# Kernel tuning notes

Hardware: AMD Instinct MI355X
Metric: run time of the kernel (lower is better)

Reference implementation:

```python
import jax, jax.numpy as jnp
import numpy as np

H, D = 2, 64          # heads, hidden_dim per head
HD = H * D            # 128
N_NODES = 50000
N_EDGES = 800000
N_GRAPHS = 64
IN_CH, EDGE_DIM, N_CLASSES = 2, 1, 30


def _tconv(x, src, dst, Wq, bq, Wk, bk, Wv, bv, We, Ws, bs):
    """PyG TransformerConv (concat=True, root_weight=True, beta=False)."""
    n = x.shape[0]
    q = (x @ Wq + bq).reshape(n, H, D)
    k = (x @ Wk + bk).reshape(n, H, D)
    v = (x @ Wv + bv).reshape(n, H, D)
    # edge embedding (lin_edge has no bias in PyG)
    return _attend(q, k, v, x @ Ws + bs, src, dst, We, n)


def _attend(q, k, v, skip, src, dst, We_e, n):
    kj = k[src] + We_e            # [E,H,D]
    vj = v[src] + We_e
    logits = (q[dst] * kj).sum(-1) / jnp.sqrt(jnp.asarray(D, q.dtype))  # [E,H]
    m = jax.ops.segment_max(logits, dst, num_segments=n)
    m = jnp.where(jnp.isfinite(m), m, jnp.zeros_like(m))
    ex = jnp.exp(logits - m[dst])
    denom = jax.ops.segment_sum(ex, dst, num_segments=n)
    alpha = ex / (denom[dst] + 1e-16)                                   # segment softmax
    agg = jax.ops.segment_sum(alpha[..., None] * vj, dst, num_segments=n)
    return agg.reshape(n, HD) + skip


def _forward(x, edge_index, edge_attr, batch,
             l0_Wq, l0_bq, l0_Wk, l0_bk, l0_Wv, l0_bv, l0_We, l0_Ws, l0_bs,
             l1_Wq, l1_bq, l1_Wk, l1_bk, l1_Wv, l1_bv, l1_We, l1_Ws, l1_bs,
             cW1, cb1, cW2, cb2):
    src, dst = edge_index[0], edge_index[1]
    e0 = (edge_attr @ l0_We).reshape(-1, H, D)
    e1 = (edge_attr @ l1_We).reshape(-1, H, D)
    n = x.shape[0]

    h = _attend((x @ l0_Wq + l0_bq).reshape(n, H, D),
                (x @ l0_Wk + l0_bk).reshape(n, H, D),
                (x @ l0_Wv + l0_bv).reshape(n, H, D),
                x @ l0_Ws + l0_bs, src, dst, e0, n)
    h = jax.nn.relu(h)
    h = _attend((h @ l1_Wq + l1_bq).reshape(n, H, D),
                (h @ l1_Wk + l1_bk).reshape(n, H, D),
                (h @ l1_Wv + l1_bv).reshape(n, H, D),
                h @ l1_Ws + l1_bs, src, dst, e1, n)
    h = jax.nn.relu(h)

    # global_mean_pool over graphs
    sums = jax.ops.segment_sum(h, batch, num_segments=N_GRAPHS)
    cnt = jax.ops.segment_sum(jnp.ones((n,), h.dtype), batch, num_segments=N_GRAPHS)
    g = sums / jnp.maximum(cnt, 1.0)[:, None]                           # [G, 128]

    return jax.nn.relu(g @ cW1 + cb1) @ cW2 + cb2                       # [G, 30]


def setup_inputs() -> dict:
    key = jax.random.key(0)
    ks = jax.random.split(key, 40)
    it = iter(ks)

    def lin(k, fan_in, fan_out):
        s = 1.0 / np.sqrt(fan_in)
        return jax.random.uniform(k, (fan_in, fan_out), jnp.float32, -s, s)

    inp = {
        'x': jax.random.normal(next(it), (N_NODES, IN_CH), jnp.float32),
        'edge_index': jax.random.randint(next(it), (2, N_EDGES), 0, N_NODES),
        'edge_attr': jax.random.normal(next(it), (N_EDGES, EDGE_DIM), jnp.float32),
        'batch': jnp.sort(jax.random.randint(next(it), (N_NODES,), 0, N_GRAPHS)),
    }
    for li, cin in (('l0', IN_CH), ('l1', HD)):
        for nm in ('Wq', 'Wk', 'Wv'):
            inp[f'{li}_{nm}'] = lin(next(it), cin, HD)
            inp[f'{li}_{nm.replace("W", "b")}'] = jax.random.uniform(
                next(it), (HD,), jnp.float32, -1 / np.sqrt(cin), 1 / np.sqrt(cin))
        inp[f'{li}_We'] = lin(next(it), EDGE_DIM, HD)
        inp[f'{li}_Ws'] = lin(next(it), cin, HD)
        inp[f'{li}_bs'] = jax.random.uniform(next(it), (HD,), jnp.float32,
                                             -1 / np.sqrt(cin), 1 / np.sqrt(cin))
    inp['cW1'] = lin(next(it), HD, 128)
    inp['cb1'] = jax.random.uniform(next(it), (128,), jnp.float32, -1 / np.sqrt(HD), 1 / np.sqrt(HD))
    inp['cW2'] = lin(next(it), 128, N_CLASSES)
    inp['cb2'] = jax.random.uniform(next(it), (N_CLASSES,), jnp.float32, -1 / np.sqrt(128), 1 / np.sqrt(128))
    return inp


def reference(x, edge_index, edge_attr, batch,
              l0_Wq, l0_bq, l0_Wk, l0_bk, l0_Wv, l0_bv, l0_We, l0_Ws, l0_bs,
              l1_Wq, l1_bq, l1_Wk, l1_bk, l1_Wv, l1_bv, l1_We, l1_Ws, l1_bs,
              cW1, cb1, cW2, cb2):
    return _forward(x, edge_index, edge_attr, batch,
                    l0_Wq, l0_bq, l0_Wk, l0_bk, l0_Wv, l0_bv, l0_We, l0_Ws, l0_bs,
                    l1_Wq, l1_bq, l1_Wk, l1_bk, l1_Wv, l1_bv, l1_We, l1_Ws, l1_bs,
                    cW1, cb1, cW2, cb2)
```

## Files before the change

### kernel.cpp

```cpp
#include <hip/hip_runtime.h>
#include <hip/hip_fp16.h>
#include <cstdint>
#include <cstddef>

#define HD 128

typedef short bf16x8 __attribute__((ext_vector_type(8)));
typedef float f32x4 __attribute__((ext_vector_type(4)));

__device__ __forceinline__ unsigned short f2bf(float f) {
    unsigned int u = __float_as_uint(f);
    u += 0x7fff + ((u >> 16) & 1);
    return (unsigned short)(u >> 16);
}
__device__ __forceinline__ float bf2f(unsigned short h) {
    return __uint_as_float(((unsigned int)h) << 16);
}

template<int CTRL>
__device__ __forceinline__ float dpp_add(float x) {
    int y = __builtin_amdgcn_update_dpp(0, __float_as_int(x), CTRL, 0xF, 0xF, true);
    return x + __int_as_float(y);
}
__device__ __forceinline__ float half_reduce(float x) {
    x = dpp_add<0xB1>(x);
    x = dpp_add<0x4E>(x);
    x = dpp_add<0x124>(x);
    x = dpp_add<0x128>(x);
    x += __shfl_xor(x, 16, 64);
    return x;
}

__device__ __forceinline__ void pair_update_s(
    float& m, float& s, float2& acc,
    float lA, float lB,
    float vAx, float vAy, float vBx, float vBy)
{
    float nm = fmaxf(fmaxf(m, lA), lB);
    float sc = __expf(m - nm);
    float eA = __expf(lA - nm);
    float eB = __expf(lB - nm);
    s     = fmaf(s, sc, eA + eB);
    acc.x = fmaf(acc.x, sc, fmaf(eA, vAx, eB * vBx));
    acc.y = fmaf(acc.y, sc, fmaf(eA, vAy, eB * vBy));
    m = nm;
}
__device__ __forceinline__ void single_update_s(
    float& m, float& s, float2& acc,
    float lg, float vx, float vy)
{
    float nm = fmaxf(m, lg);
    float sc = __expf(m - nm);
    float ex = __expf(lg - nm);
    s     = fmaf(s, sc, ex);
    acc.x = fmaf(acc.x, sc, ex * vx);
    acc.y = fmaf(acc.y, sc, ex * vy);
    m = nm;
}

__global__ __launch_bounds__(256) void hist_kernel(
    const int* __restrict__ dst, int* __restrict__ cnt, int E)
{
    int e = blockIdx.x * 256 + threadIdx.x;
    if (e < E) atomicAdd(&cnt[dst[e]], 1);
}

__global__ __launch_bounds__(256) void scanA_kernel(
    const int* __restrict__ cnt, int* __restrict__ row_ptr,
    int* __restrict__ bsum, int n)
{
    __shared__ int sdata[256];
    int t = threadIdx.x;
    int base = blockIdx.x * 512 + 2 * t;
    int a = (base < n) ? cnt[base] : 0;
    int b = (base + 1 < n) ? cnt[base + 1] : 0;
    int local = a + b;
    sdata[t] = local;
    __syncthreads();
    #pragma unroll
    for (int off = 1; off < 256; off <<= 1) {
        int val = (t >= off) ? sdata[t - off] : 0;
        __syncthreads();
        sdata[t] += val;
        __syncthreads();
    }
    int excl = sdata[t] - local;
    if (base < n)     row_ptr[base] = excl;
    if (base + 1 < n) row_ptr[base + 1] = excl + a;
    if (t == 255) bsum[blockIdx.x] = sdata[255];
}

__global__ __launch_bounds__(256) void scanB_kernel(
    const int* __restrict__ bsum, int* __restrict__ boff, int B)
{
    __shared__ int sdata[256];
    int t = threadIdx.x;
    int local = (t < B) ? bsum[t] : 0;
    sdata[t] = local;
    __syncthreads();
    #pragma unroll
    for (int off = 1; off < 256; off <<= 1) {
        int val = (t >= off) ? sdata[t - off] : 0;
        __syncthreads();
        sdata[t] += val;
        __syncthreads();
    }
    if (t < B) boff[t] = sdata[t] - local;
}

__global__ __launch_bounds__(256) void scanC_kernel(
    int* __restrict__ row_ptr, int* __restrict__ cursor,
    const int* __restrict__ boff, int n, int E)
{
    int t = threadIdx.x;
    int base = blockIdx.x * 512 + 2 * t;
    int off = boff[blockIdx.x];
    if (base + 1 < n) {
        int2 v = *(int2*)&row_ptr[base];
        v.x += off; v.y += off;
        *(int2*)&row_ptr[base] = v;
        *(int2*)&cursor[base]  = v;
    } else if (base < n) {
        int v = row_ptr[base] + off;
        row_ptr[base] = v; cursor[base] = v;
    }
    if (blockIdx.x == 0 && t == 0) row_ptr[n] = E;
}

__global__ __launch_bounds__(256) void scatter_kernel(
    const int* __restrict__ dst, const int* __restrict__ src,
    const float* __restrict__ eattr, int* __restrict__ cursor,
    int2* __restrict__ epack, int E)
{
    int e = blockIdx.x * 256 + threadIdx.x;
    if (e < E) {
        int pos = atomicAdd(&cursor[dst[e]], 1);
        epack[pos] = make_int2(src[e], __float_as_int(eattr[e]));
    }
}

__global__ __launch_bounds__(256) void attn0_kernel(
    const float* __restrict__ x,
    const float* __restrict__ Wq, const float* __restrict__ bq,
    const float* __restrict__ Wk, const float* __restrict__ bk,
    const float* __restrict__ Wv, const float* __restrict__ bv,
    const float* __restrict__ We, const float* __restrict__ Ws,
    const float* __restrict__ bs,
    const int2* __restrict__ epack, const int* __restrict__ row_ptr,
    float* __restrict__ out, int n)
{
    int i = blockIdx.x * 4 + (threadIdx.x >> 6);
    if (i >= n) return;
    int l = threadIdx.x & 63;
    int j0 = 2 * l;

    float2 wk0 = *(const float2*)&Wk[j0];
    float2 wk1 = *(const float2*)&Wk[HD + j0];
    float2 wv0 = *(const float2*)&Wv[j0];
    float2 wv1 = *(const float2*)&Wv[HD + j0];
    float2 bk2 = *(const float2*)&bk[j0];
    float2 bv2 = *(const float2*)&bv[j0];
    float2 we  = *(const float2*)&We[j0];

    float x0 = x[2 * i], x1 = x[2 * i + 1];
    float2 wq0 = *(const float2*)&Wq[j0];
    float2 wq1 = *(const float2*)&Wq[HD + j0];
    float2 bq2 = *(const float2*)&bq[j0];
    float2 q;
    q.x = fmaf(x1, wq1.x, fmaf(x0, wq0.x, bq2.x));
    q.y = fmaf(x1, wq1.y, fmaf(x0, wq0.y, bq2.y));

    float c0 = half_reduce(fmaf(q.x, wk0.x, q.y * wk0.y)) * 0.125f;
    float c1 = half_reduce(fmaf(q.x, wk1.x, q.y * wk1.y)) * 0.125f;
    float cb = half_reduce(fmaf(q.x, bk2.x, q.y * bk2.y)) * 0.125f;
    float cw = half_reduce(fmaf(q.x, we.x,  q.y * we.y))  * 0.125f;

    int p0 = __builtin_amdgcn_readfirstlane(row_ptr[i]);
    int p1 = __builtin_amdgcn_readfirstlane(row_ptr[i + 1]);

    float m = -INFINITY, s = 0.f;
    float2 acc = make_float2(0.f, 0.f);

    float2 xs0 = {}, xs1 = {}, xs2 = {}, xs3 = {};
    float ea0 = 0.f, ea1 = 0.f, ea2 = 0.f, ea3 = 0.f;

#define LD0(t, idx) do { if ((idx) < p1) { int2 ep_ = epack[idx]; \
    ea##t = __int_as_float(ep_.y); xs##t = *(const float2*)&x[2 * ep_.x]; } } while (0)

#define LOGIT0(xs, ea) fmaf(ea, cw, fmaf(xs.y, c1, fmaf(xs.x, c0, cb)))
#define VREC(xs, ea, vx, vy) \
    float vx = fmaf(ea, we.x, fmaf(xs.y, wv1.x, fmaf(xs.x, wv0.x, bv2.x))); \
    float vy = fmaf(ea, we.y, fmaf(xs.y, wv1.y, fmaf(xs.x, wv0.y, bv2.y)));

    LD0(0, p0); LD0(1, p0 + 1); LD0(2, p0 + 2); LD0(3, p0 + 3);

    int p = p0;
    for (; p + 3 < p1; p += 4) {
        float2 c0v = xs0, c1v = xs1, c2v = xs2, c3v = xs3;
        float a0 = ea0, a1 = ea1, a2 = ea2, a3 = ea3;
        LD0(0, p + 4); LD0(1, p + 5); LD0(2, p + 6); LD0(3, p + 7);
        { VREC(c0v, a0, vAx, vAy) VREC(c1v, a1, vBx, vBy)
          pair_update_s(m, s, acc, LOGIT0(c0v, a0), LOGIT0(c1v, a1), vAx, vAy, vBx, vBy); }
        { VREC(c2v, a2, vAx, vAy) VREC(c3v, a3, vBx, vBy)
          pair_update_s(m, s, acc, LOGIT0(c2v, a2), LOGIT0(c3v, a3), vAx, vAy, vBx, vBy); }
    }
    int rem = p1 - p;
    if (rem >= 2) {
        VREC(xs0, ea0, vAx, vAy) VREC(xs1, ea1, vBx, vBy)
        pair_update_s(m, s, acc, LOGIT0(xs0, ea0), LOGIT0(xs1, ea1), vAx, vAy, vBx, vBy);
    }
    if (rem == 1) {
        VREC(xs0, ea0, vx, vy)
        single_update_s(m, s, acc, LOGIT0(xs0, ea0), vx, vy);
    } else if (rem == 3) {
        VREC(xs2, ea2, vx, vy)
        single_update_s(m, s, acc, LOGIT0(xs2, ea2), vx, vy);
    }

    float inv = 1.f / (s + 1e-16f);
    float2 ws0 = *(const float2*)&Ws[j0];
    float2 ws1 = *(const float2*)&Ws[HD + j0];
    float2 bs2 = *(const float2*)&bs[j0];
    float sk_x = fmaf(x1, ws1.x, fmaf(x0, ws0.x, bs2.x));
    float sk_y = fmaf(x1, ws1.y, fmaf(x0, ws0.y, bs2.y));
    float2 res;
    res.x = fmaxf(fmaf(acc.x, inv, sk_x), 0.f);
    res.y = fmaxf(fmaf(acc.y, inv, sk_y), 0.f);
    *(float2*)&out[(size_t)i * HD + j0] = res;
}

__global__ __launch_bounds__(256) void attn_kernel(
    const __half* __restrict__ qh, const __half* __restrict__ kvh,
    const __half* __restrict__ sh, const float* __restrict__ We,
    const int2* __restrict__ epack, const int* __restrict__ row_ptr,
    float* __restrict__ out, int n)
{
    int i = blockIdx.x * 4 + (threadIdx.x >> 6);
    if (i >= n) return;
    int l = threadIdx.x & 63;
    const int2* kv8 = (const int2*)kvh;
    const __half2* qh2 = (const __half2*)qh;
    const __half2* sh2 = (const __half2*)sh;
    float2 q  = __half22float2(qh2[(size_t)i * 64 + l]);
    float2 we = *(const float2*)&We[2 * l];
    int p0 = __builtin_amdgcn_readfirstlane(row_ptr[i]);
    int p1 = __builtin_amdgcn_readfirstlane(row_ptr[i + 1]);

    float m = -INFINITY, s = 0.f;
    float2 acc = make_float2(0.f, 0.f);

    int2 kv0 = {}, kv1 = {}, kv2 = {}, kv3 = {};
    float ea0 = 0.f, ea1 = 0.f, ea2 = 0.f, ea3 = 0.f;

#define LD1(t, idx) do { if ((idx) < p1) { int2 ep_ = epack[idx]; \
    ea##t = __int_as_float(ep_.y); kv##t = kv8[(size_t)ep_.x * 64 + l]; } } while (0)

#define KVX(raw, ea, kx, ky, vx, vy) \
    float2 kf_##kx = __half22float2(*(const __half2*)&raw.x); \
    float2 vf_##kx = __half22float2(*(const __half2*)&raw.y); \
    float kx = fmaf(ea, we.x, kf_##kx.x), ky = fmaf(ea, we.y, kf_##kx.y); \
    float vx = fmaf(ea, we.x, vf_##kx.x), vy = fmaf(ea, we.y, vf_##kx.y);

    LD1(0, p0); LD1(1, p0 + 1); LD1(2, p0 + 2); LD1(3, p0 + 3);

    int p = p0;
    for (; p + 3 < p1; p += 4) {
        int2 c0 = kv0, c1 = kv1, c2 = kv2, c3 = kv3;
        float a0 = ea0, a1 = ea1, a2 = ea2, a3 = ea3;
        LD1(0, p + 4); LD1(1, p + 5); LD1(2, p + 6); LD1(3, p + 7);
        {
            KVX(c0, a0, kAx, kAy, vAx, vAy)
            KVX(c1, a1, kBx, kBy, vBx, vBy)
            float lA = half_reduce(fmaf(q.x, kAx, q.y * kAy)) * 0.125f;
            float lB = half_reduce(fmaf(q.x, kBx, q.y * kBy)) * 0.125f;
            pair_update_s(m, s, acc, lA, lB, vAx, vAy, vBx, vBy);
        }
        {
            KVX(c2, a2, kAx, kAy, vAx, vAy)
            KVX(c3, a3, kBx, kBy, vBx, vBy)
            float lA = half_reduce(fmaf(q.x, kAx, q.y * kAy)) * 0.125f;
            float lB = half_reduce(fmaf(q.x, kBx, q.y * kBy)) * 0.125f;
            pair_update_s(m, s, acc, lA, lB, vAx, vAy, vBx, vBy);
        }
    }
    int rem = p1 - p;
    if (rem >= 2) {
        KVX(kv0, ea0, kAx, kAy, vAx, vAy)
        KVX(kv1, ea1, kBx, kBy, vBx, vBy)
        float lA = half_reduce(fmaf(q.x, kAx, q.y * kAy)) * 0.125f;
        float lB = half_reduce(fmaf(q.x, kBx, q.y * kBy)) * 0.125f;
        pair_update_s(m, s, acc, lA, lB, vAx, vAy, vBx, vBy);
    }
    if (rem == 1) {
        KVX(kv0, ea0, kx, ky, vx, vy)
        single_update_s(m, s, acc, half_reduce(fmaf(q.x, kx, q.y * ky)) * 0.125f, vx, vy);
    } else if (rem == 3) {
        KVX(kv2, ea2, kx, ky, vx, vy)
        single_update_s(m, s, acc, half_reduce(fmaf(q.x, kx, q.y * ky)) * 0.125f, vx, vy);
    }

    float inv = 1.f / (s + 1e-16f);
    float2 skp = __half22float2(sh2[(size_t)i * 64 + l]);
    float2 res;
    res.x = fmaxf(fmaf(acc.x, inv, skp.x), 0.f);
    res.y = fmaxf(fmaf(acc.y, inv, skp.y), 0.f);
    *(float2*)&out[(size_t)i * HD + 2 * l] = res;
}

__global__ __launch_bounds__(256) void pack_kernel(
    const float* __restrict__ Wq, const float* __restrict__ Wk,
    const float* __restrict__ Wv, const float* __restrict__ Ws,
    const float* __restrict__ bq, const float* __restrict__ bk,
    const float* __restrict__ bv, const float* __restrict__ bs,
    unsigned short* __restrict__ Wph, unsigned short* __restrict__ Wpl,
    float* __restrict__ bias_cat)
{
    int id = blockIdx.x * 256 + threadIdx.x;
    if (id < 65536) {
        int j = id & 7, lane = (id >> 3) & 63, ks = (id >> 9) & 3, gnt = id >> 11;
        int k = ks * 32 + (lane >> 4) * 8 + j;
        int ncol = gnt * 16 + (lane & 15);
        int mat = ncol >> 7, d = ncol & 127;
        const float* W = (mat == 0) ? Wq : (mat == 1) ? Wk : (mat == 2) ? Wv : Ws;
        float w = W[k * HD + d];
        unsigned short hi = f2bf(w);
        Wph[id] = hi;
        Wpl[id] = f2bf(w - bf2f(hi));
    }
    if (id < 512) {
        int mat = id >> 7, d = id & 127;
        const float* b = (mat == 0) ? bq : (mat == 1) ? bk : (mat == 2) ? bv : bs;
        bias_cat[id] = b[d];
    }
}

__global__ __launch_bounds__(256) void lin1_mfma(
    const float* __restrict__ A,
    const unsigned short* __restrict__ Wph, const unsigned short* __restrict__ Wpl,
    const float* __restrict__ bias_cat,
    __half* __restrict__ qh, __half* __restrict__ kvh, __half* __restrict__ sh,
    int n)
{
    __shared__ float As[64 * 132];
    int tid = threadIdx.x;
    int row0 = blockIdx.x * 64;

    #pragma unroll
    for (int it = 0; it < 8; ++it) {
        int idx = it * 1024 + tid * 4;
        int r = idx >> 7, c = idx & 127;
        float4 av = make_float4(0.f, 0.f, 0.f, 0.f);
        if (row0 + r < n) av = *(const float4*)&A[(size_t)(row0 + r) * HD + c];
        *(float4*)&As[r * 132 + c] = av;
    }
    __syncthreads();

    int wave = tid >> 6, lane = tid & 63;
    int m = lane & 15, quad = lane >> 4;

    bf16x8 ah[4], al[4];
    const float* Arow = &As[(wave * 16 + m) * 132];
    #pragma unroll
    for (int ks = 0; ks < 4; ++ks) {
        float4 x0 = *(const float4*)&Arow[ks * 32 + quad * 8];
        float4 x1 = *(const float4*)&Arow[ks * 32 + quad * 8 + 4];
        float v[8] = {x0.x, x0.y, x0.z, x0.w, x1.x, x1.y, x1.z, x1.w};
        #pragma unroll
        for (int j = 0; j < 8; ++j) {
            unsigned short hi = f2bf(v[j]);
            ah[ks][j] = (short)hi;
            al[ks][j] = (short)f2bf(v[j] - bf2f(hi));
        }
    }

    const bf16x8* PH = (const bf16x8*)Wph;
    const bf16x8* PL = (const bf16x8*)Wpl;
    __half2* qh2  = (__half2*)qh;
    __half2* kvh2 = (__half2*)kvh;
    __half2* sh2  = (__half2*)sh;

    int gnt0 = blockIdx.y * 16;
    bf16x8 bhA[4], blA[4], bhB[4], blB[4];
    #pragma unroll
    for (int ks = 0; ks < 4; ++ks) {
        bhA[ks] = PH[(gnt0 * 4 + ks) * 64 + lane];
        blA[ks] = PL[(gnt0 * 4 + ks) * 64 + lane];
    }

    #pragma unroll 2
    for (int nt = 0; nt < 16; ++nt) {
        int gnt = gnt0 + nt;
        if (nt + 1 < 16) {
            #pragma unroll
            for (int ks = 0; ks < 4; ++ks) {
                bhB[ks] = PH[((gnt + 1) * 4 + ks) * 64 + lane];
                blB[ks] = PL[((gnt + 1) * 4 + ks) * 64 + lane];
            }
        }
        f32x4 acc = {0.f, 0.f, 0.f, 0.f};
        #pragma unroll
        for (int ks = 0; ks < 4; ++ks) {
            acc = __builtin_amdgcn_mfma_f32_16x16x32_bf16(ah[ks], bhA[ks], acc, 0, 0, 0);
            acc = __builtin_amdgcn_mfma_f32_16x16x32_bf16(ah[ks], blA[ks], acc, 0, 0, 0);
            acc = __builtin_amdgcn_mfma_f32_16x16x32_bf16(al[ks], bhA[ks], acc, 0, 0, 0);
        }
        int ocol = gnt * 16 + m;
        int mat = gnt >> 3;
        int d = ocol & 127;
        float bias = bias_cat[ocol];
        bool evenl = (lane & 1) == 0;
        #pragma unroll
        for (int reg = 0; reg < 4; ++reg) {
            int orow = row0 + wave * 16 + quad * 4 + reg;
            float val = acc[reg] + bias;
            float other = __shfl_xor(val, 1, 64);
            if (orow < n && evenl) {
                __half2 hv = __floats2half2_rn(val, other);
                size_t dp = (size_t)(d >> 1);
                if (mat == 0)      qh2[(size_t)orow * 64 + dp] = hv;
                else if (mat == 1) kvh2[(size_t)orow * 128 + dp * 2] = hv;
                else if (mat == 2) kvh2[(size_t)orow * 128 + dp * 2 + 1] = hv;
                else               sh2[(size_t)orow * 64 + dp] = hv;
            }
        }
        #pragma unroll
        for (int ks = 0; ks < 4; ++ks) { bhA[ks] = bhB[ks]; blA[ks] = blB[ks]; }
    }
}

__global__ __launch_bounds__(128) void pool_kernel(
    const float* __restrict__ h, const int* __restrict__ batch,
    float* __restrict__ gsums, float* __restrict__ gcnt, int n)
{
    __shared__ int sb[64];
    int i0 = blockIdx.x * 64;
    int d = threadIdx.x;
    int iend = i0 + 64; if (iend > n) iend = n;
    int csize = iend - i0;
    if (d < csize) sb[d] = batch[i0 + d];
    __syncthreads();
    if (csize <= 0) return;
    float local = 0.f;
    int cur = sb[0];
    int runc = 0;
    for (int i = i0; i < iend; ++i) {
        int g = sb[i - i0];
        if (g != cur) {
            atomicAdd(&gsums[(size_t)cur * HD + d], local);
            if (d == 0) atomicAdd(&gcnt[cur], (float)runc);
            local = 0.f; runc = 0; cur = g;
        }
        local += h[(size_t)i * HD + d];
        runc++;
    }
    atomicAdd(&gsums[(size_t)cur * HD + d], local);
    if (d == 0) atomicAdd(&gcnt[cur], (float)runc);
}

__global__ __launch_bounds__(128) void cls_kernel(
    const float* __restrict__ gsums, const float* __restrict__ gcnt,
    const float* __restrict__ cW1, const float* __restrict__ cb1,
    const float* __restrict__ cW2, const float* __restrict__ cb2,
    float* __restrict__ out)
{
    __shared__ float g[128];
    __shared__ float t[128];
    int gi = blockIdx.x, j = threadIdx.x;
    float c = fmaxf(gcnt[gi], 1.0f);
    g[j] = gsums[(size_t)gi * HD + j] / c;
    __syncthreads();
    float a = cb1[j];
    for (int k = 0; k < 128; ++k) a = fmaf(g[k], cW1[k * 128 + j], a);
    t[j] = fmaxf(a, 0.f);
    __syncthreads();
    if (j < 30) {
        float a2 = cb2[j];
        for (int k = 0; k < 128; ++k) a2 = fmaf(t[k], cW2[k * 30 + j], a2);
        out[gi * 30 + j] = a2;
    }
}

extern "C" void kernel_launch(void* const* d_in, const int* in_sizes, int n_in,
                              void* d_out, int out_size, void* d_ws, size_t ws_size,
                              hipStream_t stream)
{
    const float* x     = (const float*)d_in[0];
    const int*   ei    = (const int*)d_in[1];
    const float* eattr = (const float*)d_in[2];
    const int*   batch = (const int*)d_in[3];
    const float* l0_Wq = (const float*)d_in[4];
    const float* l0_bq = (const float*)d_in[5];
    const float* l0_Wk = (const float*)d_in[6];
    const float* l0_bk = (const float*)d_in[7];
    const float* l0_Wv = (const float*)d_in[8];
    const float* l0_bv = (const float*)d_in[9];
    const float* l0_We = (const float*)d_in[10];
    const float* l0_Ws = (const float*)d_in[11];
    const float* l0_bs = (const float*)d_in[12];
    const float* l1_Wq = (const float*)d_in[13];
    const float* l1_bq = (const float*)d_in[14];
    const float* l1_Wk = (const float*)d_in[15];
    const float* l1_bk = (const float*)d_in[16];
    const float* l1_Wv = (const float*)d_in[17];
    const float* l1_bv = (const float*)d_in[18];
    const float* l1_We = (const float*)d_in[19];
    const float* l1_Ws = (const float*)d_in[20];
    const float* l1_bs = (const float*)d_in[21];
    const float* cW1   = (const float*)d_in[22];
    const float* cb1   = (const float*)d_in[23];
    const float* cW2   = (const float*)d_in[24];
    const float* cb2   = (const float*)d_in[25];

    int n = in_sizes[0] / 2;
    int E = in_sizes[2];
    int G = out_size / 30;
    int B = (n + 511) / 512;

    size_t nd = (size_t)n * HD;
    float* h      = (float*)d_ws;
    __half* qh    = (__half*)(h + nd);
    __half* sh    = qh + nd;
    __half* kvh   = sh + nd;
    float* bias_cat = (float*)(kvh + (size_t)n * 256);
    unsigned short* Wph = (unsigned short*)(bias_cat + 512);
    unsigned short* Wpl = Wph + 65536;
    int2* epack   = (int2*)(Wpl + 65536);
    int* cnt      = (int*)(epack + E);
    int* row_ptr  = cnt + n;
    int* cursor   = row_ptr + n + 2;
    int* bsum     = cursor + n;
    int* boff     = bsum + 256;
    float* gsums  = (float*)(boff + 256);
    float* gcnt   = gsums + (size_t)G * HD;

    const int* srcI = ei;
    const int* dstI = ei + E;

    hipMemsetAsync(cnt, 0, (size_t)n * sizeof(int), stream);
    hipMemsetAsync(gsums, 0, ((size_t)G * HD + G) * sizeof(float), stream);

    hist_kernel<<<(E + 255) / 256, 256, 0, stream>>>(dstI, cnt, E);
    scanA_kernel<<<B, 256, 0, stream>>>(cnt, row_ptr, bsum, n);
    scanB_kernel<<<1, 256, 0, stream>>>(bsum, boff, B);
    scanC_kernel<<<B, 256, 0, stream>>>(row_ptr, cursor, boff, n, E);
    scatter_kernel<<<(E + 255) / 256, 256, 0, stream>>>(dstI, srcI, eattr, cursor, epack, E);

    pack_kernel<<<256, 256, 0, stream>>>(l1_Wq, l1_Wk, l1_Wv, l1_Ws,
                                         l1_bq, l1_bk, l1_bv, l1_bs,
                                         Wph, Wpl, bias_cat);

    attn0_kernel<<<(n + 3) / 4, 256, 0, stream>>>(
        x, l0_Wq, l0_bq, l0_Wk, l0_bk, l0_Wv, l0_bv, l0_We, l0_Ws, l0_bs,
        epack, row_ptr, h, n);

    lin1_mfma<<<dim3((n + 63) / 64, 2), 256, 0, stream>>>(
        h, Wph, Wpl, bias_cat, qh, kvh, sh, n);
    attn_kernel<<<(n + 3) / 4, 256, 0, stream>>>(
        qh, kvh, sh, l1_We, epack, row_ptr, h, n);

    pool_kernel<<<(n + 63) / 64, 128, 0, stream>>>(h, batch, gsums, gcnt, n);
    cls_kernel<<<G, 128, 0, stream>>>(gsums, gcnt, cW1, cb1, cW2, cb2, (float*)d_out);
}
```

Measured before the change: 414.0 us.

## Enlarge lin1 MFMA tile to 128 rows, swizzle LDS, stage KV output

Each lin1_mfma block now covers 128 rows, with every wave computing two 16-row subtiles so each loaded weight fragment feeds twice as many MFMAs. The LDS A tile uses an XOR swizzle in place of padding to avoid bank conflicts. Column tiles are reassigned so one y-block produces Q and skip while the other produces K and V. The interleaved KV output is staged in LDS and written with coalesced float4 stores instead of scattered half2 writes. Grid size halves, which lowers occupancy and parallelism, and the loop unroll pragma was dropped.

```diff
diff --git a/kernel.cpp b/kernel.cpp
--- a/kernel.cpp
+++ b/kernel.cpp
@@ -341,91 +341,134 @@
     __half* __restrict__ qh, __half* __restrict__ kvh, __half* __restrict__ sh,
     int n)
 {
-    __shared__ float As[64 * 132];
+    __shared__ float As[128 * 128];
     int tid = threadIdx.x;
-    int row0 = blockIdx.x * 64;
+    int row0 = blockIdx.x * 128;
+    int yb = blockIdx.y;
 
     #pragma unroll
-    for (int it = 0; it < 8; ++it) {
-        int idx = it * 1024 + tid * 4;
+    for (int it = 0; it < 16; ++it) {
+        int idx = (it * 256 + tid) * 4;
         int r = idx >> 7, c = idx & 127;
         float4 av = make_float4(0.f, 0.f, 0.f, 0.f);
         if (row0 + r < n) av = *(const float4*)&A[(size_t)(row0 + r) * HD + c];
-        *(float4*)&As[r * 132 + c] = av;
+        int sl = (c >> 2) ^ (r & 7);
+        *(float4*)&As[r * 128 + sl * 4] = av;
     }
     __syncthreads();
 
     int wave = tid >> 6, lane = tid & 63;
     int m = lane & 15, quad = lane >> 4;
 
-    bf16x8 ah[4], al[4];
-    const float* Arow = &As[(wave * 16 + m) * 132];
+    bf16x8 ah[2][4], al[2][4];
     #pragma unroll
-    for (int ks = 0; ks < 4; ++ks) {
-        float4 x0 = *(const float4*)&Arow[ks * 32 + quad * 8];
-        float4 x1 = *(const float4*)&Arow[ks * 32 + quad * 8 + 4];
-        float v[8] = {x0.x, x0.y, x0.z, x0.w, x1.x, x1.y, x1.z, x1.w};
+    for (int sub = 0; sub < 2; ++sub) {
+        int r = wave * 32 + sub * 16 + m;
+        const float* base = &As[r * 128];
+        int sw = r & 7;
         #pragma unroll
-        for (int j = 0; j < 8; ++j) {
-            unsigned short hi = f2bf(v[j]);
-            ah[ks][j] = (short)hi;
-            al[ks][j] = (short)f2bf(v[j] - bf2f(hi));
-        }
-    }
+        for (int ks = 0; ks < 4; ++ks) {
+            int i40 = (ks * 8 + quad * 2) ^ sw;
+            int i41 = (ks * 8 + quad * 2 + 1) ^ sw;
+            float4 x0 = *(const float4*)&base[i40 * 4];
+            float4 x1 = *(const float4*)&base[i41 * 4];
+            float v[8] = {x0.x, x0.y, x0.z, x0.w, x1.x, x1.y, x1.z, x1.w};
+            #pragma unroll
+            for (int j = 0; j < 8; ++j) {
+                unsigned short hi = f2bf(v[j]);
+                ah[sub][ks][j] = (short)hi;
+                al[sub][ks][j] = (short)f2bf(v[j] - bf2f(hi));
+            }
+        }
+    }
+    __syncthreads();
 
     const bf16x8* PH = (const bf16x8*)Wph;
     const bf16x8* PL = (const bf16x8*)Wpl;
-    __half2* qh2  = (__half2*)qh;
-    __half2* kvh2 = (__half2*)kvh;
-    __half2* sh2  = (__half2*)sh;
-
-    int gnt0 = blockIdx.y * 16;
+    __half2* qh2 = (__half2*)qh;
+    __half2* sh2 = (__half2*)sh;
+    __half*  kvS = (__half*)As;
+
+    #define GNT_OF(nt) ((yb == 0) ? (((nt) < 8) ? (nt) : (nt) + 16) : (nt) + 8)
+
     bf16x8 bhA[4], blA[4], bhB[4], blB[4];
-    #pragma unroll
-    for (int ks = 0; ks < 4; ++ks) {
-        bhA[ks] = PH[(gnt0 * 4 + ks) * 64 + lane];
-        blA[ks] = PL[(gnt0 * 4 + ks) * 64 + lane];
-    }
-
-    #pragma unroll 2
+    {
+        int g0 = GNT_OF(0);
+        #pragma unroll
+        for (int ks = 0; ks < 4; ++ks) {
+            bhA[ks] = PH[(g0 * 4 + ks) * 64 + lane];
+            blA[ks] = PL[(g0 * 4 + ks) * 64 + lane];
+        }
+    }
+
     for (int nt = 0; nt < 16; ++nt) {
-        int gnt = gnt0 + nt;
+        int gnt = GNT_OF(nt);
         if (nt + 1 < 16) {
+            int g2 = GNT_OF(nt + 1);
             #pragma unroll
             for (int ks = 0; ks < 4; ++ks) {
-                bhB[ks] = PH[((gnt + 1) * 4 + ks) * 64 + lane];
-                blB[ks] = PL[((gnt + 1) * 4 + ks) * 64 + lane];
+                bhB[ks] = PH[(g2 * 4 + ks) * 64 + lane];
+                blB[ks] = PL[(g2 * 4 + ks) * 64 + lane];
             }
         }
-        f32x4 acc = {0.f, 0.f, 0.f, 0.f};
+        f32x4 acc0 = {0.f, 0.f, 0.f, 0.f};
+        f32x4 acc1 = {0.f, 0.f, 0.f, 0.f};
         #pragma unroll
         for (int ks = 0; ks < 4; ++ks) {
-            acc = __builtin_amdgcn_mfma_f32_16x16x32_bf16(ah[ks], bhA[ks], acc, 0, 0, 0);
-            acc = __builtin_amdgcn_mfma_f32_16x16x32_bf16(ah[ks], blA[ks], acc, 0, 0, 0);
-            acc = __builtin_amdgcn_mfma_f32_16x16x32_bf16(al[ks], bhA[ks], acc, 0, 0, 0);
+            acc0 = __builtin_amdgcn_mfma_f32_16x16x32_bf16(ah[0][ks], bhA[ks], acc0, 0, 0, 0);
+            acc1 = __builtin_amdgcn_mfma_f32_16x16x32_bf16(ah[1][ks], bhA[ks], acc1, 0, 0, 0);
+            acc0 = __builtin_amdgcn_mfma_f32_16x16x32_bf16(ah[0][ks], blA[ks], acc0, 0, 0, 0);
+            acc1 = __builtin_amdgcn_mfma_f32_16x16x32_bf16(ah[1][ks], blA[ks], acc1, 0, 0, 0);
+            acc0 = __builtin_amdgcn_mfma_f32_16x16x32_bf16(al[0][ks], bhA[ks], acc0, 0, 0, 0);
+            acc1 = __builtin_amdgcn_mfma_f32_16x16x32_bf16(al[1][ks], bhA[ks], acc1, 0, 0, 0);
         }
         int ocol = gnt * 16 + m;
-        int mat = gnt >> 3;
         int d = ocol & 127;
         float bias = bias_cat[ocol];
-        bool evenl = (lane & 1) == 0;
-        #pragma unroll
-        for (int reg = 0; reg < 4; ++reg) {
-            int orow = row0 + wave * 16 + quad * 4 + reg;
-            float val = acc[reg] + bias;
-            float other = __shfl_xor(val, 1, 64);
-            if (orow < n && evenl) {
-                __half2 hv = __floats2half2_rn(val, other);
-                size_t dp = (size_t)(d >> 1);
-                if (mat == 0)      qh2[(size_t)orow * 64 + dp] = hv;
-                else if (mat == 1) kvh2[(size_t)orow * 128 + dp * 2] = hv;
-                else if (mat == 2) kvh2[(size_t)orow * 128 + dp * 2 + 1] = hv;
-                else               sh2[(size_t)orow * 64 + dp] = hv;
+        if (yb == 0) {
+            __half2* dst = (gnt < 8) ? qh2 : sh2;
+            bool evenl = (m & 1) == 0;
+            #pragma unroll
+            for (int sub = 0; sub < 2; ++sub) {
+                f32x4 acc = sub ? acc1 : acc0;
+                #pragma unroll
+                for (int reg = 0; reg < 4; ++reg) {
+                    int orow = row0 + wave * 32 + sub * 16 + quad * 4 + reg;
+                    float val = acc[reg] + bias;
+                    float other = __shfl_xor(val, 1, 64);
+                    if (orow < n && evenl)
+                        dst[(size_t)orow * 64 + (d >> 1)] = __floats2half2_rn(val, other);
+                }
+            }
+        } else {
+            int slot = 4 * (d >> 1) + (d & 1) + ((gnt >= 16) ? 2 : 0);
+            #pragma unroll
+            for (int sub = 0; sub < 2; ++sub) {
+                f32x4 acc = sub ? acc1 : acc0;
+                #pragma unroll
+                for (int reg = 0; reg < 4; ++reg) {
+                    int row_l = wave * 32 + sub * 16 + quad * 4 + reg;
+                    kvS[row_l * 256 + slot] = __float2half(acc[reg] + bias);
+                }
             }
         }
         #pragma unroll
         for (int ks = 0; ks < 4; ++ks) { bhA[ks] = bhB[ks]; blA[ks] = blB[ks]; }
     }
+
+    if (yb == 1) {
+        __syncthreads();
+        const float4* kvS4 = (const float4*)kvS;
+        float4* kvh4 = (float4*)kvh;
+        #pragma unroll
+        for (int it = 0; it < 16; ++it) {
+            int idx = it * 256 + tid;
+            int row = idx >> 5, c4 = idx & 31;
+            if (row0 + row < n)
+                kvh4[(size_t)(row0 + row) * 32 + c4] = kvS4[row * 32 + c4];
+        }
+    }
+    #undef GNT_OF
 }
 
 __global__ __launch_bounds__(128) void pool_kernel(
@@ -553,7 +596,7 @@
         x, l0_Wq, l0_bq, l0_Wk, l0_bk, l0_Wv, l0_bv, l0_We, l0_Ws, l0_bs,
         epack, row_ptr, h, n);
 
-    lin1_mfma<<<dim3((n + 63) / 64, 2), 256, 0, stream>>>(
+    lin1_mfma<<<dim3((n + 127) / 128, 2), 256, 0, stream>>>(
         h, Wph, Wpl, bias_cat, qh, kvh, sh, n);
     attn_kernel<<<(n + 3) / 4, 256, 0, stream>>>(
         qh, kvh, sh, l1_We, epack, row_ptr, h, n);
```

Measured after the change: 392.2 us. 1.06x faster.
